# Optimization experiments

Measured on AMD Instinct MI355X. Metric: run time of the kernel, lower is better.

The kernel has to match this reference:

```python
import jax, jax.numpy as jnp
import numpy as np

B, T, D_IN, E, H = 2, 2048, 1024, 64, 16  # batch, num_tokens, input dim, emb_size(per-head), num_heads


def setup_inputs() -> dict:
    key = jax.random.key(0)
    ks = jax.random.split(key, 6)
    s = 0.02
    inp = jax.random.normal(ks[0], (B, T, D_IN), dtype=jnp.float32)
    # causal mask: 1.0 where attention is disallowed (j > i), matching `scaled_compat -= mask * 1e9`
    mask = jnp.triu(jnp.ones((T, T), dtype=jnp.float32), k=1)
    Wq = jax.random.normal(ks[1], (D_IN, E * H), dtype=jnp.float32) * s
    Wk = jax.random.normal(ks[2], (D_IN, E * H), dtype=jnp.float32) * s
    Wv = jax.random.normal(ks[3], (D_IN, E * H), dtype=jnp.float32) * s
    Wu = jax.random.normal(ks[4], (E * H, E), dtype=jnp.float32) * s
    bu = jnp.zeros((E,), dtype=jnp.float32)
    return {"inp": inp, "mask": mask, "Wq": Wq, "Wk": Wk, "Wv": Wv, "Wu": Wu, "bu": bu}


def reference(inp, mask, Wq, Wk, Wv, Wu, bu):
    b = inp.shape[0]
    q = inp @ Wq  # [B,T,E*H]
    k = inp @ Wk
    v = inp @ Wv
    # NOTE: original reshapes last dim as (E, H) -> heads on fastest axis (interleaved layout)
    q = q.reshape(b, T, E, H)
    k = k.reshape(b, T, E, H)
    v = v.reshape(b, T, E, H)
    scores = jnp.einsum("bteh,bseh->bhts", q, k) / jnp.sqrt(jnp.float32(E))  # [B,H,T,T]
    if mask is not None:
        scores = scores - mask * 1e9
    attn = jax.nn.softmax(scores, axis=-1)
    wv = jnp.einsum("bhts,bseh->bhte", attn, v)  # [B,H,T,E]
    # transpose [0,2,3,1] -> [B,T,E,H], then flatten to [B,T,E*H] (H fastest, matching original)
    wv = jnp.transpose(wv, (0, 2, 3, 1)).reshape(b, T, E * H)
    return wv @ Wu + bu  # unify Dense(emb_size), with bias
```

## Files before the change

### kernel.cpp

```cpp
#include <hip/hip_runtime.h>


typedef __bf16 bf16x8 __attribute__((ext_vector_type(8)));
typedef float f32x4 __attribute__((ext_vector_type(4)));
typedef unsigned short u16;
typedef unsigned int u32;

#define AS1 __attribute__((address_space(1)))
#define AS3 __attribute__((address_space(3)))

__device__ __forceinline__ void gll16(const void* g, void* l) {
    __builtin_amdgcn_global_load_lds((const AS1 u32*)g, (AS3 u32*)l, 16, 0, 0);
}

__device__ __forceinline__ u16 f2bf(float f) {
    union { float f; u32 u; } v; v.f = f;
    u32 r = (v.u + 0x7FFFu + ((v.u >> 16) & 1u)) >> 16;
    return (u16)r;
}

#define MM 4096
#define SCALE_LOG2E 0.18033688011112042f

__global__ void cast_x(const float* __restrict__ in, u16* __restrict__ out, int n4) {
    int i = blockIdx.x * blockDim.x + threadIdx.x;
    if (i < n4) {
        float4 f = ((const float4*)in)[i];
        ushort4 o;
        o.x = f2bf(f.x); o.y = f2bf(f.y); o.z = f2bf(f.z); o.w = f2bf(f.w);
        ((ushort4*)out)[i] = o;
    }
}

__global__ void transpose_w(const float* __restrict__ Wq, const float* __restrict__ Wk,
                            const float* __restrict__ Wv, const float* __restrict__ Wu,
                            u16* __restrict__ wqt, u16* __restrict__ wkt,
                            u16* __restrict__ wvt, u16* __restrict__ wut) {
    int z = blockIdx.z;
    const float* src; u16* dst; int N;
    if (z == 0)      { src = Wq; dst = wqt; N = 1024; }
    else if (z == 1) { src = Wk; dst = wkt; N = 1024; }
    else if (z == 2) { src = Wv; dst = wvt; N = 1024; }
    else             { src = Wu; dst = wut; N = 64; if (blockIdx.y >= 2) return; }
    __shared__ float lds[32][33];
    int k0 = blockIdx.x * 32, n0 = blockIdx.y * 32;
    int tid = threadIdx.x;
    int c = tid & 31, r0 = tid >> 5;
#pragma unroll
    for (int p = 0; p < 4; ++p) {
        int r = r0 + p * 8;
        lds[r][c] = src[(k0 + r) * N + n0 + c];
    }
    __syncthreads();
#pragma unroll
    for (int p = 0; p < 4; ++p) {
        int n = n0 + r0 + p * 8;
        if (z < 3) {
            int rnew = ((n & 15) << 6) | (n >> 4);
            dst[rnew * 1024 + k0 + c] = f2bf(lds[c][n - n0]);
        } else {
            int k = k0 + c;
            int kp = ((k & 15) << 6) | (k >> 4);
            dst[n * 1024 + kp] = f2bf(lds[c][n - n0]);
        }
    }
}

__global__ __launch_bounds__(256) void gemm_qkv(const u16* __restrict__ xb,
                                                const u16* __restrict__ wqt,
                                                const u16* __restrict__ wkt,
                                                const u16* __restrict__ wvt,
                                                u16* __restrict__ qh, u16* __restrict__ kh,
                                                u16* __restrict__ vh) {
    int z = blockIdx.z;
    const u16* wt = (z == 0) ? wqt : (z == 1) ? wkt : wvt;
    u16* dst      = (z == 0) ? qh  : (z == 1) ? kh  : vh;
    __shared__ u16 lA[2][128 * 32];
    __shared__ u16 lB[2][128 * 32];
    int tid = threadIdx.x;
    int m0 = blockIdx.x * 128, n0 = blockIdx.y * 128;
    int lane = tid & 63, w = tid >> 6;
    int wr = w >> 1, wc = w & 1;
    int l15 = lane & 15, quad = lane >> 4;
    f32x4 acc[4][4] = {};
    int srow = tid >> 2, scol = (tid & 3) * 8;
    const u16* ga = xb + (m0 + srow) * 1024 + scol;
    const u16* gb = wt + (n0 + srow) * 1024 + scol;
#pragma unroll
    for (int pp = 0; pp < 2; ++pp) {
        gll16(ga + pp * 65536, lA[0] + (pp * 256 + tid) * 8);
        gll16(gb + pp * 65536, lB[0] + (pp * 256 + tid) * 8);
    }
#pragma unroll 1
    for (int kk = 0; kk < 32; ++kk) {
        int cur = kk & 1;
        asm volatile("s_waitcnt vmcnt(0)" ::: "memory");
        __builtin_amdgcn_s_barrier();
        if (kk + 1 < 32) {
            int kb = (kk + 1) * 32;
#pragma unroll
            for (int pp = 0; pp < 2; ++pp) {
                gll16(ga + pp * 65536 + kb, lA[cur ^ 1] + (pp * 256 + tid) * 8);
                gll16(gb + pp * 65536 + kb, lB[cur ^ 1] + (pp * 256 + tid) * 8);
            }
        }
        bf16x8 af[4], bfr[4];
#pragma unroll
        for (int i = 0; i < 4; ++i)
            af[i] = *(const bf16x8*)(lA[cur] + (wr * 64 + i * 16 + l15) * 32 + quad * 8);
#pragma unroll
        for (int j = 0; j < 4; ++j)
            bfr[j] = *(const bf16x8*)(lB[cur] + (wc * 64 + j * 16 + l15) * 32 + quad * 8);
#pragma unroll
        for (int i = 0; i < 4; ++i)
#pragma unroll
            for (int j = 0; j < 4; ++j)
                acc[i][j] = __builtin_amdgcn_mfma_f32_16x16x32_bf16(af[i], bfr[j], acc[i][j], 0, 0, 0);
    }
    int bb = m0 >> 11;
    int hb = (n0 >> 6) + wc;
    if (z < 2) {
        float scale = (z == 0) ? SCALE_LOG2E : 1.f;
#pragma unroll
        for (int i = 0; i < 4; ++i)
#pragma unroll
            for (int j = 0; j < 4; ++j)
#pragma unroll
                for (int r = 0; r < 4; ++r) {
                    int m = m0 + wr * 64 + i * 16 + quad * 4 + r;
                    dst[m * 1024 + hb * 64 + j * 16 + l15] = f2bf(acc[i][j][r] * scale);
                }
    } else {
#pragma unroll
        for (int j = 0; j < 4; ++j)
#pragma unroll
            for (int r = 0; r < 4; ++r) {
                ushort4 o;
                o.x = f2bf(acc[0][j][r]); o.y = f2bf(acc[1][j][r]);
                o.z = f2bf(acc[2][j][r]); o.w = f2bf(acc[3][j][r]);
                *(ushort4*)(dst + (((bb * 16 + hb) * 64) + j * 16 + l15) * 2048 +
                            (m0 & 2047) + wr * 64 + (quad * 4 + r) * 4) = o;
            }
    }
}

__global__ __launch_bounds__(256) void attn(const u16* __restrict__ qh, const u16* __restrict__ kh,
                                            const u16* __restrict__ vh, u16* __restrict__ ot,
                                            float* __restrict__ part, float* __restrict__ lp) {
    __shared__ u16 smem[17408];
    u16* sPQ = smem;
    u16* sK = smem + 9216;
    u16* sV = smem + 13312;
    const int tid = threadIdx.x;
    const int lane = tid & 63, w = tid >> 6;
    const int quad = lane >> 4, l15 = lane & 15;
    const int s = blockIdx.x, by = blockIdx.y;
    int qt, j0, j1, half;
    if (s < 8)       { qt = 7 - s;  j0 = 0;      j1 = 2 * qt + 2; half = -1; }
    else if (s < 16) { qt = s;      j0 = 0;      j1 = qt + 1;     half = 0;  }
    else             { qt = s - 8;  j0 = qt + 1; j1 = 2 * qt + 2; half = 1;  }
    const int b = by >> 4, h = by & 15;
    const u16* kbase = kh + (b * 2048) * 1024 + h * 64;
    const u16* vbase = vh + (by * 64) * 2048;
    const int c0 = tid, c1 = 256 + tid;
    const int r0c = c0 >> 3, o0c = (c0 & 7) * 8;
    const int r1c = c1 >> 3, o1c = (c1 & 7) * 8;
    const int sw0 = ((r0c >> 1) & 3) << 3;
    const int sw1 = ((r1c >> 1) & 3) << 3;
    u16* sKd0 = sK + (o0c >> 5) * 2048 + r0c * 32 + ((o0c & 31) ^ sw0);
    u16* sKd1 = sK + (o1c >> 5) * 2048 + r1c * 32 + ((o1c & 31) ^ sw1);
    u16* sVd0 = sV + (o0c >> 5) * 2048 + r0c * 32 + ((o0c & 31) ^ sw0);
    u16* sVd1 = sV + (o1c >> 5) * 2048 + r1c * 32 + ((o1c & 31) ^ sw1);
    const u16* kg0 = kbase + r0c * 1024 + o0c;
    const u16* kg1 = kbase + r1c * 1024 + o1c;
    const u16* vg0 = vbase + r0c * 2048 + o0c;
    const u16* vg1 = vbase + r1c * 2048 + o1c;
    const int qsw = (quad ^ ((l15 >> 1) & 3)) * 8;

    const u16* qg = qh + (b * 2048 + qt * 128) * 1024 + h * 64;
#pragma unroll
    for (int p = 0; p < 4; ++p) {
        int c = p * 256 + tid;
        gll16(qg + (c >> 3) * 1024 + (c & 7) * 8, sPQ + c * 8);
    }
    __syncthreads();
    bf16x8 aq[2][2];
#pragma unroll
    for (int rg = 0; rg < 2; ++rg)
#pragma unroll
        for (int k2 = 0; k2 < 2; ++k2)
            aq[rg][k2] = *(const bf16x8*)(sPQ + (w * 32 + rg * 16 + l15) * 64 + k2 * 32 + quad * 8);

    float lpart[2][4] = {};
    f32x4 oacc[2][4] = {};
    uint4 kr0 = *(const uint4*)(kg0 + j0 * 65536);
    uint4 kr1 = *(const uint4*)(kg1 + j0 * 65536);
    uint4 vr0 = *(const uint4*)(vg0 + j0 * 64);
    uint4 vr1 = *(const uint4*)(vg1 + j0 * 64);
    u16* sPw = sPQ + w * 2304;
    for (int jt = j0; jt < j1; ++jt) {
        __syncthreads();
        *(uint4*)sKd0 = kr0; *(uint4*)sKd1 = kr1;
        *(uint4*)sVd0 = vr0; *(uint4*)sVd1 = vr1;
        __syncthreads();
        if (jt + 1 < j1) {
            kr0 = *(const uint4*)(kg0 + (jt + 1) * 65536);
            kr1 = *(const uint4*)(kg1 + (jt + 1) * 65536);
            vr0 = *(const uint4*)(vg0 + (jt + 1) * 64);
            vr1 = *(const uint4*)(vg1 + (jt + 1) * 64);
        }
        f32x4 sacc[2][4] = {};
#pragma unroll
        for (int j4 = 0; j4 < 4; ++j4)
#pragma unroll
            for (int k2 = 0; k2 < 2; ++k2) {
                bf16x8 bk = *(const bf16x8*)(sK + k2 * 2048 + (j4 * 16 + l15) * 32 + qsw);
                sacc[0][j4] = __builtin_amdgcn_mfma_f32_16x16x32_bf16(aq[0][k2], bk, sacc[0][j4], 0, 0, 0);
                sacc[1][j4] = __builtin_amdgcn_mfma_f32_16x16x32_bf16(aq[1][k2], bk, sacc[1][j4], 0, 0, 0);
            }
        if (jt >= 2 * qt) {
            int soff = (jt - 2 * qt) * 64;
#pragma unroll
            for (int rg = 0; rg < 2; ++rg)
#pragma unroll
                for (int j4 = 0; j4 < 4; ++j4)
#pragma unroll
                    for (int r = 0; r < 4; ++r) {
                        int sg = soff + j4 * 16 + l15;
                        int tg = w * 32 + rg * 16 + quad * 4 + r;
                        if (sg > tg) sacc[rg][j4][r] = -1e30f;
                    }
        }
#pragma unroll
        for (int rg = 0; rg < 2; ++rg)
#pragma unroll
            for (int j4 = 0; j4 < 4; ++j4)
#pragma unroll
                for (int r = 0; r < 4; ++r) {
                    float pe = __builtin_amdgcn_exp2f(sacc[rg][j4][r]);
                    sacc[rg][j4][r] = pe;
                    lpart[rg][r] += pe;
                }
#pragma unroll
        for (int rg = 0; rg < 2; ++rg)
#pragma unroll
            for (int r = 0; r < 4; ++r) {
                ushort4 o;
                o.x = f2bf(sacc[rg][0][r]); o.y = f2bf(sacc[rg][1][r]);
                o.z = f2bf(sacc[rg][2][r]); o.w = f2bf(sacc[rg][3][r]);
                *(ushort4*)(sPw + (rg * 16 + quad * 4 + r) * 72 + l15 * 4) = o;
            }
        bf16x8 ap[2][2];
#pragma unroll
        for (int rg = 0; rg < 2; ++rg)
#pragma unroll
            for (int k2 = 0; k2 < 2; ++k2)
                ap[rg][k2] = *(const bf16x8*)(sPw + (rg * 16 + l15) * 72 + k2 * 32 + quad * 8);
#pragma unroll
        for (int e4 = 0; e4 < 4; ++e4)
#pragma unroll
            for (int k2 = 0; k2 < 2; ++k2) {
                bf16x8 bv = *(const bf16x8*)(sV + k2 * 2048 + (e4 * 16 + l15) * 32 + qsw);
                oacc[0][e4] = __builtin_amdgcn_mfma_f32_16x16x32_bf16(ap[0][k2], bv, oacc[0][e4], 0, 0, 0);
                oacc[1][e4] = __builtin_amdgcn_mfma_f32_16x16x32_bf16(ap[1][k2], bv, oacc[1][e4], 0, 0, 0);
            }
    }
    if (half < 0) {
#pragma unroll
        for (int rg = 0; rg < 2; ++rg)
#pragma unroll
            for (int r = 0; r < 4; ++r) {
                float rs = lpart[rg][r];
#pragma unroll
                for (int off = 1; off < 16; off <<= 1) rs += __shfl_xor(rs, off, 16);
                float inv = 1.f / rs;
                int t = qt * 128 + w * 32 + rg * 16 + quad * 4 + r;
                int base = (b * 2048 + t) * 1024 + h * 64;
#pragma unroll
                for (int e4 = 0; e4 < 4; ++e4)
                    ot[base + e4 * 16 + l15] = f2bf(oacc[rg][e4][r] * inv);
            }
    } else {
        int pb = by * 8 + (qt - 8);
        float* pg = part + (pb * 2 + half) * 8192;
        float* lg = lp + pb * 256 + half * 128;
#pragma unroll
        for (int rg = 0; rg < 2; ++rg)
#pragma unroll
            for (int r = 0; r < 4; ++r) {
                float rs = lpart[rg][r];
#pragma unroll
                for (int off = 1; off < 16; off <<= 1) rs += __shfl_xor(rs, off, 16);
                int row = w * 32 + rg * 16 + quad * 4 + r;
                if (l15 == 0) lg[row] = rs;
#pragma unroll
                for (int e4 = 0; e4 < 4; ++e4)
                    pg[row * 64 + e4 * 16 + l15] = oacc[rg][e4][r];
            }
    }
}

__global__ __launch_bounds__(256) void combine_o(const float* __restrict__ part,
                                                 const float* __restrict__ lp,
                                                 u16* __restrict__ ot) {
    int pb = blockIdx.x, tid = threadIdx.x;
    int by = pb >> 3, qt = 8 + (pb & 7);
    int b = by >> 4, h = by & 15;
    const float* pA = part + pb * 16384;
    const float* pB = pA + 8192;
    const float* lA = lp + pb * 256;
    const float* lB = lA + 128;
#pragma unroll
    for (int p = 0; p < 8; ++p) {
        int e = p * 1024 + tid * 4;
        int row = e >> 6, col = e & 63;
        float4 a = *(const float4*)(pA + e);
        float4 c = *(const float4*)(pB + e);
        float inv = 1.f / (lA[row] + lB[row]);
        int t = qt * 128 + row;
        ushort4 o;
        o.x = f2bf((a.x + c.x) * inv); o.y = f2bf((a.y + c.y) * inv);
        o.z = f2bf((a.z + c.z) * inv); o.w = f2bf((a.w + c.w) * inv);
        *(ushort4*)(ot + (b * 2048 + t) * 1024 + h * 64 + col) = o;
    }
}

__global__ __launch_bounds__(256) void gemm_out(const u16* __restrict__ ot, const u16* __restrict__ wut,
                                                const float* __restrict__ bu, float* __restrict__ out) {
    __shared__ float red[4][1088];
    int tid = threadIdx.x, lane = tid & 63, w = tid >> 6;
    int quad = lane >> 4, l15 = lane & 15;
    int m0 = blockIdx.x * 16;
    f32x4 acc[4] = {};
    const u16* aptr = ot + (m0 + l15) * 1024 + w * 256 + quad * 8;
    const u16* bptr = wut + l15 * 1024 + w * 256 + quad * 8;
#pragma unroll
    for (int kk = 0; kk < 8; ++kk) {
        bf16x8 af = *(const bf16x8*)(aptr + kk * 32);
#pragma unroll
        for (int j = 0; j < 4; ++j) {
            bf16x8 bfr = *(const bf16x8*)(bptr + j * 16 * 1024 + kk * 32);
            acc[j] = __builtin_amdgcn_mfma_f32_16x16x32_bf16(af, bfr, acc[j], 0, 0, 0);
        }
    }
#pragma unroll
    for (int j = 0; j < 4; ++j)
#pragma unroll
        for (int r = 0; r < 4; ++r)
            red[w][(j * 16 + l15) * 17 + quad * 4 + r] = acc[j][r];
    __syncthreads();
    int n = tid & 63, mq = tid >> 6;
    float bias = bu[n];
#pragma unroll
    for (int i = 0; i < 4; ++i) {
        int m = mq * 4 + i;
        float s = red[0][n * 17 + m] + red[1][n * 17 + m] + red[2][n * 17 + m] + red[3][n * 17 + m];
        out[(m0 + m) * 64 + n] = s + bias;
    }
}

#define OFF_XB   0u
#define OFF_WQT  8388608u
#define OFF_WKT  10485760u
#define OFF_WVT  12582912u
#define OFF_WUT  14680064u
#define OFF_QH   14811136u
#define OFF_KH   23199744u
#define OFF_VH   31588352u
#define OFF_OT   OFF_XB
#define OFF_PART 39976960u
#define OFF_LP   56754176u

extern "C" void kernel_launch(void* const* d_in, const int* in_sizes, int n_in,
                              void* d_out, int out_size, void* d_ws, size_t ws_size,
                              hipStream_t stream) {
    (void)in_sizes; (void)n_in; (void)out_size; (void)ws_size;
    const float* inp = (const float*)d_in[0];
    const float* Wq = (const float*)d_in[2];
    const float* Wk = (const float*)d_in[3];
    const float* Wv = (const float*)d_in[4];
    const float* Wu = (const float*)d_in[5];
    const float* bu = (const float*)d_in[6];
    float* out = (float*)d_out;
    char* ws = (char*)d_ws;
    u16* xb  = (u16*)(ws + OFF_XB);
    u16* wqt = (u16*)(ws + OFF_WQT);
    u16* wkt = (u16*)(ws + OFF_WKT);
    u16* wvt = (u16*)(ws + OFF_WVT);
    u16* wut = (u16*)(ws + OFF_WUT);
    u16* qh  = (u16*)(ws + OFF_QH);
    u16* kh  = (u16*)(ws + OFF_KH);
    u16* vh  = (u16*)(ws + OFF_VH);
    u16* ot  = (u16*)(ws + OFF_OT);
    float* part = (float*)(ws + OFF_PART);
    float* lpw  = (float*)(ws + OFF_LP);

    cast_x<<<4096, 256, 0, stream>>>(inp, xb, (MM * 1024) / 4);
    transpose_w<<<dim3(32, 32, 4), 256, 0, stream>>>(Wq, Wk, Wv, Wu, wqt, wkt, wvt, wut);
    gemm_qkv<<<dim3(32, 8, 3), 256, 0, stream>>>(xb, wqt, wkt, wvt, qh, kh, vh);
    attn<<<dim3(24, 32), 256, 0, stream>>>(qh, kh, vh, ot, part, lpw);
    combine_o<<<256, 256, 0, stream>>>(part, lpw, ot);
    gemm_out<<<256, 256, 0, stream>>>(ot, wut, bu, out);
}
```

Measured before the change: 195.4 us.

## Double-buffer K/V tiles in LDS using direct global-to-LDS loads

Replaces register-staged K/V prefetch (global→VGPR→LDS with two barriers per tile) with global_load_lds DMA into a double-buffered LDS region. This removes one barrier and the register round trip per iteration, so the next tile's load can overlap the current tile's compute. It also changes the LDS layout to row-major 64-wide rows with an XOR swizzle on 8-element chunks, applied on the global source addresses. LDS use grows from about 34KB to 50KB per block, which may reduce occupancy.

```diff
diff --git a/kernel.cpp b/kernel.cpp
--- a/kernel.cpp
+++ b/kernel.cpp
@@ -147,10 +147,8 @@
 __global__ __launch_bounds__(256) void attn(const u16* __restrict__ qh, const u16* __restrict__ kh,
                                             const u16* __restrict__ vh, u16* __restrict__ ot,
                                             float* __restrict__ part, float* __restrict__ lp) {
-    __shared__ u16 smem[17408];
+    __shared__ u16 smem[25600];
     u16* sPQ = smem;
-    u16* sK = smem + 9216;
-    u16* sV = smem + 13312;
     const int tid = threadIdx.x;
     const int lane = tid & 63, w = tid >> 6;
     const int quad = lane >> 4, l15 = lane & 15;
@@ -160,22 +158,11 @@
     else if (s < 16) { qt = s;      j0 = 0;      j1 = qt + 1;     half = 0;  }
     else             { qt = s - 8;  j0 = qt + 1; j1 = 2 * qt + 2; half = 1;  }
     const int b = by >> 4, h = by & 15;
-    const u16* kbase = kh + (b * 2048) * 1024 + h * 64;
-    const u16* vbase = vh + (by * 64) * 2048;
-    const int c0 = tid, c1 = 256 + tid;
-    const int r0c = c0 >> 3, o0c = (c0 & 7) * 8;
-    const int r1c = c1 >> 3, o1c = (c1 & 7) * 8;
-    const int sw0 = ((r0c >> 1) & 3) << 3;
-    const int sw1 = ((r1c >> 1) & 3) << 3;
-    u16* sKd0 = sK + (o0c >> 5) * 2048 + r0c * 32 + ((o0c & 31) ^ sw0);
-    u16* sKd1 = sK + (o1c >> 5) * 2048 + r1c * 32 + ((o1c & 31) ^ sw1);
-    u16* sVd0 = sV + (o0c >> 5) * 2048 + r0c * 32 + ((o0c & 31) ^ sw0);
-    u16* sVd1 = sV + (o1c >> 5) * 2048 + r1c * 32 + ((o1c & 31) ^ sw1);
-    const u16* kg0 = kbase + r0c * 1024 + o0c;
-    const u16* kg1 = kbase + r1c * 1024 + o1c;
-    const u16* vg0 = vbase + r0c * 2048 + o0c;
-    const u16* vg1 = vbase + r1c * 2048 + o1c;
-    const int qsw = (quad ^ ((l15 >> 1) & 3)) * 8;
+    const int row0 = tid >> 3;
+    const int cb0 = (tid & 7) ^ (row0 & 7);
+    const u16* kg0 = kh + (b * 2048) * 1024 + h * 64 + row0 * 1024 + cb0 * 8;
+    const u16* vg0 = vh + (by * 64) * 2048 + row0 * 2048 + cb0 * 8;
+    const int fsw = (l15 & 7) * 8;
 
     const u16* qg = qh + (b * 2048 + qt * 128) * 1024 + h * 64;
 #pragma unroll
@@ -191,30 +178,37 @@
         for (int k2 = 0; k2 < 2; ++k2)
             aq[rg][k2] = *(const bf16x8*)(sPQ + (w * 32 + rg * 16 + l15) * 64 + k2 * 32 + quad * 8);
 
+    {
+        u16* sK0 = smem + 9216;
+        u16* sV0 = smem + 17408;
+        gll16(kg0 + j0 * 65536,         sK0 + tid * 8);
+        gll16(kg0 + j0 * 65536 + 32768, sK0 + (256 + tid) * 8);
+        gll16(vg0 + j0 * 64,            sV0 + tid * 8);
+        gll16(vg0 + j0 * 64 + 65536,    sV0 + (256 + tid) * 8);
+    }
     float lpart[2][4] = {};
     f32x4 oacc[2][4] = {};
-    uint4 kr0 = *(const uint4*)(kg0 + j0 * 65536);
-    uint4 kr1 = *(const uint4*)(kg1 + j0 * 65536);
-    uint4 vr0 = *(const uint4*)(vg0 + j0 * 64);
-    uint4 vr1 = *(const uint4*)(vg1 + j0 * 64);
     u16* sPw = sPQ + w * 2304;
     for (int jt = j0; jt < j1; ++jt) {
-        __syncthreads();
-        *(uint4*)sKd0 = kr0; *(uint4*)sKd1 = kr1;
-        *(uint4*)sVd0 = vr0; *(uint4*)sVd1 = vr1;
-        __syncthreads();
+        int cur = (jt - j0) & 1;
+        u16* sK = smem + 9216 + cur * 4096;
+        u16* sV = smem + 17408 + cur * 4096;
+        asm volatile("s_waitcnt vmcnt(0)" ::: "memory");
+        __builtin_amdgcn_s_barrier();
         if (jt + 1 < j1) {
-            kr0 = *(const uint4*)(kg0 + (jt + 1) * 65536);
-            kr1 = *(const uint4*)(kg1 + (jt + 1) * 65536);
-            vr0 = *(const uint4*)(vg0 + (jt + 1) * 64);
-            vr1 = *(const uint4*)(vg1 + (jt + 1) * 64);
+            u16* sKn = smem + 9216 + (cur ^ 1) * 4096;
+            u16* sVn = smem + 17408 + (cur ^ 1) * 4096;
+            gll16(kg0 + (jt + 1) * 65536,         sKn + tid * 8);
+            gll16(kg0 + (jt + 1) * 65536 + 32768, sKn + (256 + tid) * 8);
+            gll16(vg0 + (jt + 1) * 64,            sVn + tid * 8);
+            gll16(vg0 + (jt + 1) * 64 + 65536,    sVn + (256 + tid) * 8);
         }
         f32x4 sacc[2][4] = {};
 #pragma unroll
         for (int j4 = 0; j4 < 4; ++j4)
 #pragma unroll
             for (int k2 = 0; k2 < 2; ++k2) {
-                bf16x8 bk = *(const bf16x8*)(sK + k2 * 2048 + (j4 * 16 + l15) * 32 + qsw);
+                bf16x8 bk = *(const bf16x8*)(sK + (j4 * 16 + l15) * 64 + (((k2 * 4 + quad) * 8) ^ fsw));
                 sacc[0][j4] = __builtin_amdgcn_mfma_f32_16x16x32_bf16(aq[0][k2], bk, sacc[0][j4], 0, 0, 0);
                 sacc[1][j4] = __builtin_amdgcn_mfma_f32_16x16x32_bf16(aq[1][k2], bk, sacc[1][j4], 0, 0, 0);
             }
@@ -260,7 +254,7 @@
         for (int e4 = 0; e4 < 4; ++e4)
 #pragma unroll
             for (int k2 = 0; k2 < 2; ++k2) {
-                bf16x8 bv = *(const bf16x8*)(sV + k2 * 2048 + (e4 * 16 + l15) * 32 + qsw);
+                bf16x8 bv = *(const bf16x8*)(sV + (e4 * 16 + l15) * 64 + (((k2 * 4 + quad) * 8) ^ fsw));
                 oacc[0][e4] = __builtin_amdgcn_mfma_f32_16x16x32_bf16(ap[0][k2], bv, oacc[0][e4], 0, 0, 0);
                 oacc[1][e4] = __builtin_amdgcn_mfma_f32_16x16x32_bf16(ap[1][k2], bv, oacc[1][e4], 0, 0, 0);
             }
```

Measured after the change: 178.8 us. -8.5%, faster.
